# Kernel tuning notes

Measured on AMD Instinct MI355X. Metric: run time of the kernel, lower is better.

Reference implementation:

```python
import jax, jax.numpy as jnp
import numpy as np

B, T_IN, N, F_EMB = 64, 48, 64, 64
MAX_LEN = 64
H1 = 128   # rnn_1 hidden
H2 = 128   # rnn_2 hidden
HL = 128   # attribute_rnn (LSTM head) hidden
EMB = 32
VOCAB = 40
NC = 33    # len(unique_activities) + 1
IN_LSTM = H2 + EMB * 4  # rnn_2 + emb*(3 + attribute_number=1)


def setup_inputs():
    key = jax.random.key(0)
    ks = jax.random.split(key, 20)
    s = 0.05
    return {
        'concatenation': jax.random.normal(ks[0], (B, T_IN, N, F_EMB), jnp.float32),
        'A_in': jax.random.uniform(ks[1], (B, N, N), jnp.float32),
        'last_places_activated': jax.random.randint(ks[2], (B, 1), 0, N),
        'multiple_outputs': 0,
        'X_attributes': jax.random.randint(ks[3], (B, T_IN, 4), 0, 34),
        # GGRNN_1 (graph-gated GRU) params
        'W1': jax.random.normal(ks[4], (F_EMB, 3 * H1), jnp.float32) * s,
        'U1': jax.random.normal(ks[5], (H1, 3 * H1), jnp.float32) * s,
        'b1': jnp.zeros((3 * H1,), jnp.float32),
        # GGRNN_2 params
        'W2': jax.random.normal(ks[6], (H1, 3 * H2), jnp.float32) * s,
        'U2': jax.random.normal(ks[7], (H2, 3 * H2), jnp.float32) * s,
        'b2': jnp.zeros((3 * H2,), jnp.float32),
        # graph_embedder embedding tables
        'E_act': jax.random.normal(ks[8], (VOCAB, EMB), jnp.float32) * s,
        'E_t1': jax.random.normal(ks[9], (VOCAB, EMB), jnp.float32) * s,
        'E_t2': jax.random.normal(ks[10], (VOCAB, EMB), jnp.float32) * s,
        'E_attr': jax.random.normal(ks[11], (VOCAB, EMB), jnp.float32) * s,
        # LSTMHead params (1 layer LSTM + linear classifier)
        'Wx': jax.random.normal(ks[12], (IN_LSTM, 4 * HL), jnp.float32) * s,
        'Wh': jax.random.normal(ks[13], (HL, 4 * HL), jnp.float32) * s,
        'bl': jnp.zeros((4 * HL,), jnp.float32),
        'Wo': jax.random.normal(ks[14], (HL, NC), jnp.float32) * s,
        'bo': jnp.zeros((NC,), jnp.float32),
    }


def _ggrnn(x, A, W, U, b):
    # x: [B,T,N,F]; graph message passing (A @ x_t) feeding a per-node GRU over time
    H = U.shape[0]
    def step(h, x_t):              # h, x_t: [B,N,*]
        m = jnp.einsum('bij,bjf->bif', A, x_t)
        gx = m @ W + b             # [B,N,3H]
        gh = h @ U
        z = jax.nn.sigmoid(gx[..., :H] + gh[..., :H])
        r = jax.nn.sigmoid(gx[..., H:2 * H] + gh[..., H:2 * H])
        n = jnp.tanh(gx[..., 2 * H:] + r * gh[..., 2 * H:])
        h_new = (1.0 - z) * n + z * h
        return h_new, h_new
    h0 = jnp.zeros((x.shape[0], x.shape[2], H), x.dtype)
    _, hs = jax.lax.scan(step, h0, jnp.moveaxis(x, 1, 0))
    return jnp.moveaxis(hs, 0, 1)  # return_sequences -> [B,T,N,H]


def _lstm_head(x, Wx, Wh, b, Wo, bo):
    # x: [B,T,D] -> last hidden -> logits [B,NC]
    H = Wh.shape[0]
    def step(carry, x_t):
        h, c = carry
        g = x_t @ Wx + h @ Wh + b  # [B,4H]
        i = jax.nn.sigmoid(g[:, :H])
        f = jax.nn.sigmoid(g[:, H:2 * H])
        gg = jnp.tanh(g[:, 2 * H:3 * H])
        o = jax.nn.sigmoid(g[:, 3 * H:])
        c = f * c + i * gg
        h = o * jnp.tanh(c)
        return (h, c), None
    init = (jnp.zeros((x.shape[0], H), x.dtype), jnp.zeros((x.shape[0], H), x.dtype))
    (h, _), _ = jax.lax.scan(step, init, jnp.moveaxis(x, 1, 0))
    return h @ Wo + bo


def reference(concatenation, A_in, last_places_activated, multiple_outputs, X_attributes,
              W1, U1, b1, W2, U2, b2, E_act, E_t1, E_t2, E_attr, Wx, Wh, bl, Wo, bo):
    # zero-pad time dim at the FRONT to max_len (ZeroPad2d after permute)
    pad_t = MAX_LEN - concatenation.shape[1]
    x = jnp.pad(concatenation, ((0, 0), (pad_t, 0), (0, 0), (0, 0)))
    x = _ggrnn(x, A_in, W1, U1, b1)     # [B,T,N,H1]
    x = _ggrnn(x, A_in, W2, U2, b2)     # [B,T,N,H2]
    # the nested python loop reverses time, max-pools over nodes, and re-inserts at
    # the front, which exactly preserves time order -> plain segment max over N
    pooled = jnp.max(x, axis=2)         # [B,T,H2]
    # attribute embeddings (zero-index padding at the front of time)
    pad_a = MAX_LEN - X_attributes.shape[1]
    attrs = jnp.pad(X_attributes, ((0, 0), (pad_a, 0), (0, 0)))
    emb = jnp.concatenate([E_act[attrs[..., 0]], E_t1[attrs[..., 1]],
                           E_t2[attrs[..., 2]], E_attr[attrs[..., 3]]], axis=-1)
    seq = jnp.concatenate([pooled, emb], axis=-1)  # [B,T,H2+4*EMB]
    logits = _lstm_head(seq, Wx, Wh, bl, Wo, bo)   # [B,NC]
    return logits
```

## Files before the change

### kernel.cpp

```cpp
#include <hip/hip_runtime.h>
#include <hip/hip_bf16.h>
#include <cstdint>


#define BB 64
#define TIN 48
#define TPAD 16
#define G3 384
#define NC 33
#define HL4 512

using u16 = unsigned short;
using u32 = unsigned int;
using bf16x8 = __attribute__((ext_vector_type(8))) short;
using f32x4  = __attribute__((ext_vector_type(4))) float;

__device__ __forceinline__ float b2f(u16 u) {
    u32 x = ((u32)u) << 16; float f; __builtin_memcpy(&f, &x, 4); return f;
}
__device__ __forceinline__ u16 f2b(float f) {
    u32 x; __builtin_memcpy(&x, &f, 4);
    u32 r = (x + 0x7fffu + ((x >> 16) & 1u)) >> 16;
    return (u16)r;
}
__device__ __forceinline__ float sigm(float x) { return 1.f / (1.f + __expf(-x)); }
__device__ __forceinline__ float tanh_f(float x) {
    float e = __expf(2.f * x);
    return 1.f - 2.f / (e + 1.f);
}
__device__ __forceinline__ u32 encf(float f) {
    int i = __float_as_int(f);
    return (i < 0) ? ~(u32)i : ((u32)i | 0x80000000u);
}
__device__ __forceinline__ float decf(u32 u) {
    int i = (u & 0x80000000u) ? (int)(u & 0x7fffffffu) : ~(int)u;
    return __int_as_float(i);
}

__global__ __launch_bounds__(256) void prep_kernel(
        const float* __restrict__ A, const float* __restrict__ U1,
        const float* __restrict__ U2, const float* __restrict__ W1,
        const float* __restrict__ W2, const float* __restrict__ Wx,
        u16* __restrict__ ah, u16* __restrict__ al,
        u16* __restrict__ uth1, u16* __restrict__ uth2,
        u16* __restrict__ wth1, u16* __restrict__ wth2,
        u16* __restrict__ wxth, u16* __restrict__ wxtl) {
    int blk = blockIdx.x, tid = threadIdx.x;
    if (blk < 1024) {
        int idx = blk * 256 + tid;
        float f = A[idx];
        int bi = idx >> 6, j = idx & 63;
        int o = (bi << 6) + (j ^ ((bi & 7) << 3));
        u16 h = f2b(f); ah[o] = h; al[o] = f2b(f - b2f(h));
    } else if (blk < 1216) {
        int idx = (blk - 1024) * 256 + tid;
        int k = idx & 127, col = idx >> 7;
        uth1[col * 128 + k] = f2b(U1[(size_t)k * G3 + col]);
    } else if (blk < 1408) {
        int idx = (blk - 1216) * 256 + tid;
        int k = idx & 127, col = idx >> 7;
        uth2[col * 128 + k] = f2b(U2[(size_t)k * G3 + col]);
    } else if (blk < 1504) {
        int idx = (blk - 1408) * 256 + tid;
        int col = idx % 384, k = idx / 384;
        wth1[(size_t)col * 64 + k] = f2b(W1[(size_t)k * 384 + col]);
    } else if (blk < 1696) {
        int idx = (blk - 1504) * 256 + tid;
        int col = idx % 384, k = idx / 384;
        wth2[(size_t)col * 128 + k] = f2b(W2[(size_t)k * 384 + col]);
    } else {
        int idx = (blk - 1696) * 256 + tid;
        int col = idx & 511, k = idx >> 9;
        float f = Wx[(size_t)k * HL4 + col];
        u16 h = f2b(f);
        wxth[(size_t)col * 256 + k] = h;
        wxtl[(size_t)col * 256 + k] = f2b(f - b2f(h));
    }
}

template<int F>
__global__ __launch_bounds__(256, 4) void bmm_kernel(
        const u16* __restrict__ ah, const u16* __restrict__ al,
        const float* __restrict__ x1, const u16* __restrict__ h1,
        u16* __restrict__ mh, int T, int TPB) {
    __shared__ __align__(16) u16 Xs[F * 64];
    __shared__ float txf[(F == 64) ? 64 : 1][(F == 64) ? 65 : 1];
    __shared__ u16 txh[(F == 128) ? 64 : 1][(F == 128) ? 136 : 1];
    const int blk = blockIdx.x;
    const int b = blk & 63, tg0 = (blk >> 6) * TPB;
    const int tid = threadIdx.x;
    const int w = tid >> 6, l = tid & 63, lr = l & 15, lk = l >> 4;

    bf16x8 afh[2], afl[2];
    {
        int row = w * 16 + lr;
        #pragma unroll
        for (int ks = 0; ks < 2; ++ks) {
            int idx = (b << 12) + row * 64 + ((ks * 32 + lk * 8) ^ ((row & 7) << 3));
            afh[ks] = *(const bf16x8*)&ah[idx];
            afl[ks] = *(const bf16x8*)&al[idx];
        }
    }

    for (int it = 0; it < TPB; ++it) {
        const int tl = tg0 + it;
        __syncthreads();
        if constexpr (F == 64) {
            const float* in = x1 + (size_t)(b * TIN + tl) * 4096;
            for (int idx = tid; idx < 4096; idx += 256)
                txf[idx >> 6][idx & 63] = in[idx];
        } else {
            const uint4* in = (const uint4*)(h1 + (size_t)(b * TIN + tl) * 8192);
            for (int idx = tid; idx < 1024; idx += 256) {
                int j = idx >> 4, c8 = idx & 15;
                *(uint4*)&txh[j][c8 * 8] = in[idx];
            }
        }
        __syncthreads();
        if constexpr (F == 64) {
            #pragma unroll
            for (int it2 = 0; it2 < 2; ++it2) {
                int f = it2 * 32 + (tid >> 3), cc = tid & 7;
                int jb = (cc ^ (f & 7)) * 8;
                u16 tmp[8];
                #pragma unroll
                for (int jj = 0; jj < 8; ++jj) tmp[jj] = f2b(txf[jb + jj][f]);
                *(uint4*)&Xs[f * 64 + cc * 8] = *(uint4*)tmp;
            }
        } else {
            #pragma unroll
            for (int it2 = 0; it2 < 4; ++it2) {
                int d = it2 * 32 + (tid >> 3), cc = tid & 7;
                int jb = (cc ^ (d & 7)) * 8;
                u16 tmp[8];
                #pragma unroll
                for (int jj = 0; jj < 8; ++jj) tmp[jj] = txh[jb + jj][d];
                *(uint4*)&Xs[d * 64 + cc * 8] = *(uint4*)tmp;
            }
        }
        __syncthreads();

        constexpr int NCT = F / 16;
        f32x4 macc[NCT];
        #pragma unroll
        for (int ct = 0; ct < NCT; ++ct) macc[ct] = (f32x4){0.f, 0.f, 0.f, 0.f};
        #pragma unroll
        for (int ct = 0; ct < NCT; ++ct) {
            int f = ct * 16 + lr;
            #pragma unroll
            for (int ks = 0; ks < 2; ++ks) {
                bf16x8 xf = *(const bf16x8*)&Xs[f * 64 + ((ks * 32 + lk * 8) ^ ((f & 7) << 3))];
                macc[ct] = __builtin_amdgcn_mfma_f32_16x16x32_bf16(afh[ks], xf, macc[ct], 0, 0, 0);
                macc[ct] = __builtin_amdgcn_mfma_f32_16x16x32_bf16(afl[ks], xf, macc[ct], 0, 0, 0);
            }
        }
        u16* oh = mh + (size_t)(b * T + tl) * 64 * F;
        #pragma unroll
        for (int ct = 0; ct < NCT; ++ct)
            #pragma unroll
            for (int q = 0; q < 4; ++q) {
                int row = w * 16 + lk * 4 + q;
                int col = ct * 16 + lr;
                oh[row * F + col] = f2b(macc[ct][q]);
            }
    }
}

template<int F, bool POOL>
__global__ __launch_bounds__(512, 2) void scan_mfma_kernel(
        const u16* __restrict__ mh, const u16* __restrict__ uth,
        const u16* __restrict__ wth, const float* __restrict__ bias,
        u16* __restrict__ hout, u32* __restrict__ pooled, int S) {
    constexpr int KS = F / 32;
    constexpr int RQ = F / 8;
    __shared__ u16 hhi[2][16][136];
    __shared__ u16 msh[2][16][F + 8];
    const int tid = threadIdx.x;
    const int wave = tid >> 6, l = tid & 63;
    const int lr = l & 15, lk = l >> 4;
    const int blk = blockIdx.x;
    const int b = blk & 63;
    const int n0 = (blk >> 6) * 16;
    const int d = wave * 16 + lr;

    bf16x8 ub[3][4], wbh[3][KS];
    float bias3[3];
    #pragma unroll
    for (int g = 0; g < 3; ++g) {
        int col = g * 128 + d;
        #pragma unroll
        for (int ks = 0; ks < 4; ++ks)
            ub[g][ks] = *(const bf16x8*)&uth[col * 128 + ks * 32 + lk * 8];
        #pragma unroll
        for (int ks = 0; ks < KS; ++ks)
            wbh[g][ks] = *(const bf16x8*)&wth[(size_t)col * F + ks * 32 + lk * 8];
        bias3[g] = bias[col];
    }

    float hold[4] = {0.f, 0.f, 0.f, 0.f};
    #pragma unroll
    for (int q = 0; q < 4; ++q)
        hhi[0][lk * 4 + q][d] = 0;
    if (tid < 16 * RQ) {
        int row = tid / RQ, c8 = tid % RQ;
        uint4 v = *(const uint4*)&mh[((size_t)(b * S) * 64 + n0 + row) * F + c8 * 8];
        *(uint4*)&msh[0][row][c8 * 8] = v;
    }
    __syncthreads();

    for (int s = 0; s < S; ++s) {
        uint4 tv;
        const bool have = (s + 1 < S);
        if (have && tid < 16 * RQ) {
            int row = tid / RQ, c8 = tid % RQ;
            tv = *(const uint4*)&mh[((size_t)(b * S + s + 1) * 64 + n0 + row) * F + c8 * 8];
        }
        if (!POOL && s >= 1 && tid < 256) {
            int dr = tid >> 4, kb = tid & 15;
            uint4 v = *(const uint4*)&hhi[s & 1][dr][kb * 8];
            *(uint4*)(hout + ((size_t)(b * TIN + s - 1) * 64 + n0 + dr) * 128 + kb * 8) = v;
        }
        __builtin_amdgcn_s_setprio(1);
        f32x4 gxa[3];
        #pragma unroll
        for (int g = 0; g < 3; ++g)
            gxa[g] = (f32x4){bias3[g], bias3[g], bias3[g], bias3[g]};
        #pragma unroll
        for (int ks = 0; ks < KS; ++ks) {
            bf16x8 mhf = *(const bf16x8*)&msh[s & 1][lr][ks * 32 + lk * 8];
            #pragma unroll
            for (int g = 0; g < 3; ++g)
                gxa[g] = __builtin_amdgcn_mfma_f32_16x16x32_bf16(mhf, wbh[g][ks], gxa[g], 0, 0, 0);
        }
        f32x4 acc[3];
        acc[0] = acc[1] = acc[2] = (f32x4){0.f, 0.f, 0.f, 0.f};
        #pragma unroll
        for (int ks = 0; ks < 4; ++ks) {
            bf16x8 ahh = *(const bf16x8*)&hhi[s & 1][lr][ks * 32 + lk * 8];
            #pragma unroll
            for (int g = 0; g < 3; ++g)
                acc[g] = __builtin_amdgcn_mfma_f32_16x16x32_bf16(ahh, ub[g][ks], acc[g], 0, 0, 0);
        }
        __builtin_amdgcn_s_setprio(0);
        #pragma unroll
        for (int q = 0; q < 4; ++q) {
            float z  = sigm(gxa[0][q] + acc[0][q]);
            float r2 = sigm(gxa[1][q] + acc[1][q]);
            float nn = tanh_f(gxa[2][q] + r2 * acc[2][q]);
            float h = (1.f - z) * nn + z * hold[q];
            hold[q] = h;
            hhi[(s + 1) & 1][lk * 4 + q][d] = f2b(h);
        }
        if (POOL) {
            float mx = fmaxf(fmaxf(hold[0], hold[1]), fmaxf(hold[2], hold[3]));
            mx = fmaxf(mx, __shfl_xor(mx, 16, 64));
            mx = fmaxf(mx, __shfl_xor(mx, 32, 64));
            if (lk == 0)
                atomicMax(&pooled[((size_t)(b * 64 + TPAD + s)) * 128 + d], encf(mx));
        }
        if (have && tid < 16 * RQ) {
            int row = tid / RQ, c8 = tid % RQ;
            *(uint4*)&msh[(s + 1) & 1][row][c8 * 8] = tv;
        }
        __syncthreads();
    }

    if (!POOL && tid < 256) {
        int dr = tid >> 4, kb = tid & 15;
        uint4 v = *(const uint4*)&hhi[S & 1][dr][kb * 8];
        *(uint4*)(hout + ((size_t)(b * TIN + S - 1) * 64 + n0 + dr) * 128 + kb * 8) = v;
    }
}

__global__ __launch_bounds__(256, 2) void seqgemm_kernel(
        const u32* __restrict__ pooled, const int* __restrict__ xattr,
        const float* __restrict__ Ea, const float* __restrict__ E1,
        const float* __restrict__ E2, const float* __restrict__ E3,
        const u16* __restrict__ wxth, const u16* __restrict__ wxtl,
        const float* __restrict__ bl, float* __restrict__ gxl) {
    __shared__ __align__(16) u16 Ss[64 * 256];
    const int b = blockIdx.x;
    const int r0 = b * 64;
    const int c0 = blockIdx.y * 256;
    const int tid = threadIdx.x;
    const int w = tid >> 6, l = tid & 63, lr = l & 15, lk = l >> 4;
    const uint4* p4 = (const uint4*)pooled;
    for (int i = tid; i < 2048; i += 256) {
        int t = i >> 5, c4 = i & 31;
        uint4 e = p4[((size_t)(b * 64 + t)) * 32 + c4];
        u16 tmp[4];
        if (t < TPAD) { tmp[0] = tmp[1] = tmp[2] = tmp[3] = 0; }
        else {
            tmp[0] = f2b(decf(e.x)); tmp[1] = f2b(decf(e.y));
            tmp[2] = f2b(decf(e.z)); tmp[3] = f2b(decf(e.w));
        }
        *(uint2*)&Ss[t * 256 + ((c4 * 4) ^ ((t & 7) << 3))] = *(uint2*)tmp;
    }
    {
        int t = tid >> 2, tbl = tid & 3;
        int idx = (t >= TPAD) ? xattr[((size_t)(b * TIN + t - TPAD)) * 4 + tbl] : 0;
        const float* E = (tbl == 0) ? Ea : (tbl == 1) ? E1 : (tbl == 2) ? E2 : E3;
        const float4* E4 = (const float4*)(E + idx * 32);
        #pragma unroll
        for (int j = 0; j < 8; ++j) {
            float4 ev = E4[j];
            u16 tmp[4] = {f2b(ev.x), f2b(ev.y), f2b(ev.z), f2b(ev.w)};
            int col = 128 + tbl * 32 + j * 4;
            *(uint2*)&Ss[t * 256 + (col ^ ((t & 7) << 3))] = *(uint2*)tmp;
        }
    }
    __syncthreads();
    f32x4 acc[4][4];
    #pragma unroll
    for (int rt = 0; rt < 4; ++rt)
        #pragma unroll
        for (int ct = 0; ct < 4; ++ct) acc[rt][ct] = (f32x4){0.f, 0.f, 0.f, 0.f};
    const int cw = c0 + w * 64;
    #pragma unroll
    for (int ks = 0; ks < 8; ++ks) {
        bf16x8 af[4];
        #pragma unroll
        for (int rt = 0; rt < 4; ++rt) {
            int row = rt * 16 + lr;
            af[rt] = *(const bf16x8*)&Ss[row * 256 + ((ks * 32 + lk * 8) ^ ((row & 7) << 3))];
        }
        #pragma unroll
        for (int ct = 0; ct < 4; ++ct) {
            int col = cw + ct * 16 + lr;
            bf16x8 wfh = *(const bf16x8*)&wxth[(size_t)col * 256 + ks * 32 + lk * 8];
            bf16x8 wfl = *(const bf16x8*)&wxtl[(size_t)col * 256 + ks * 32 + lk * 8];
            #pragma unroll
            for (int rt = 0; rt < 4; ++rt) {
                acc[rt][ct] = __builtin_amdgcn_mfma_f32_16x16x32_bf16(af[rt], wfh, acc[rt][ct], 0, 0, 0);
                acc[rt][ct] = __builtin_amdgcn_mfma_f32_16x16x32_bf16(af[rt], wfl, acc[rt][ct], 0, 0, 0);
            }
        }
    }
    #pragma unroll
    for (int ct = 0; ct < 4; ++ct) {
        int col = cw + ct * 16 + lr;
        float bv = bl[col];
        #pragma unroll
        for (int rt = 0; rt < 4; ++rt)
            #pragma unroll
            for (int q = 0; q < 4; ++q) {
                int row = r0 + rt * 16 + lk * 4 + q;
                gxl[(size_t)row * HL4 + col] = acc[rt][ct][q] + bv;
            }
    }
}

__global__ __launch_bounds__(1024) void lstm_kernel(
        const float* __restrict__ gxl, const float* __restrict__ Wh,
        const float* __restrict__ Wo, const float* __restrict__ bo,
        float* __restrict__ out) {
    __shared__ float hsd[128];
    __shared__ __align__(16) float part[8][128][4];
    int b = blockIdx.x; int tid = threadIdx.x;
    int kq = tid >> 7, d = tid & 127;
    float w[4][16];
    #pragma unroll
    for (int g = 0; g < 4; ++g)
        #pragma unroll
        for (int kk = 0; kk < 16; ++kk)
            w[g][kk] = Wh[(size_t)(kq * 16 + kk) * HL4 + g * 128 + d];
    float c = 0.f;
    float gl[4];
    if (tid < 128) {
        hsd[tid] = 0.f;
        #pragma unroll
        for (int g = 0; g < 4; ++g)
            gl[g] = gxl[((size_t)(b * 64)) * HL4 + g * 128 + d];
    }
    __syncthreads();
    for (int t = 0; t < 64; ++t) {
        float a[4] = {0.f, 0.f, 0.f, 0.f};
        #pragma unroll
        for (int k4 = 0; k4 < 4; ++k4) {
            float4 hv = *(const float4*)&hsd[kq * 16 + k4 * 4];
            #pragma unroll
            for (int g = 0; g < 4; ++g) {
                a[g] += hv.x * w[g][k4 * 4 + 0] + hv.y * w[g][k4 * 4 + 1]
                      + hv.z * w[g][k4 * 4 + 2] + hv.w * w[g][k4 * 4 + 3];
            }
        }
        if (kq) {
            float4 pv = {a[0], a[1], a[2], a[3]};
            *(float4*)&part[kq][d][0] = pv;
        }
        __syncthreads();
        if (kq == 0) {
            float gsum[4] = {a[0], a[1], a[2], a[3]};
            #pragma unroll
            for (int q = 1; q < 8; ++q) {
                float4 v = *(const float4*)&part[q][d][0];
                gsum[0] += v.x; gsum[1] += v.y; gsum[2] += v.z; gsum[3] += v.w;
            }
            #pragma unroll
            for (int g = 0; g < 4; ++g) gsum[g] += gl[g];
            if (t + 1 < 64) {
                #pragma unroll
                for (int g = 0; g < 4; ++g)
                    gl[g] = gxl[((size_t)(b * 64 + t + 1)) * HL4 + g * 128 + d];
            }
            float ii = sigm(gsum[0]), ff = sigm(gsum[1]);
            float gg = tanh_f(gsum[2]), oo = sigm(gsum[3]);
            c = ff * c + ii * gg;
            hsd[d] = oo * tanh_f(c);
        }
        __syncthreads();
    }
    if (tid < NC) {
        float accv = bo[tid];
        for (int k = 0; k < 128; ++k) accv += hsd[k] * Wo[k * NC + tid];
        out[b * NC + tid] = accv;
    }
}

extern "C" void kernel_launch(void* const* d_in, const int* in_sizes, int n_in,
                              void* d_out, int out_size, void* d_ws, size_t ws_size,
                              hipStream_t stream) {
    const float* x  = (const float*)d_in[0];
    const float* A  = (const float*)d_in[1];
    const int* xattr = (const int*)d_in[4];
    const float* W1 = (const float*)d_in[5];
    const float* U1 = (const float*)d_in[6];
    const float* b1 = (const float*)d_in[7];
    const float* W2 = (const float*)d_in[8];
    const float* U2 = (const float*)d_in[9];
    const float* b2 = (const float*)d_in[10];
    const float* Ea = (const float*)d_in[11];
    const float* E1 = (const float*)d_in[12];
    const float* E2 = (const float*)d_in[13];
    const float* E3 = (const float*)d_in[14];
    const float* Wx = (const float*)d_in[15];
    const float* Wh = (const float*)d_in[16];
    const float* bl = (const float*)d_in[17];
    const float* Wo = (const float*)d_in[18];
    const float* bo = (const float*)d_in[19];
    float* out = (float*)d_out;
    char* ws = (char*)d_ws;
    u16* mh      = (u16*)(ws);
    u16* h1      = (u16*)(ws + 50331648);
    float* gxl   = (float*)(ws + 100663296);
    u16* a_hi    = (u16*)(ws + 109051904);
    u16* a_lo    = (u16*)(ws + 109576192);
    u16* wth1    = (u16*)(ws + 110100480);
    u16* wth2    = (u16*)(ws + 110149632);
    u16* uth1    = (u16*)(ws + 110247936);
    u16* uth2    = (u16*)(ws + 110346240);
    u16* wxth    = (u16*)(ws + 110444544);
    u16* wxtl    = (u16*)(ws + 110706688);
    u32* pooled  = (u32*)(ws + 110968832);

    prep_kernel<<<2208, 256, 0, stream>>>(A, U1, U2, W1, W2, Wx,
        a_hi, a_lo, uth1, uth2, wth1, wth2, wxth, wxtl);
    hipMemsetAsync(pooled, 0, 2097152, stream);

    bmm_kernel<64><<<BB * 12, 256, 0, stream>>>(a_hi, a_lo, x, nullptr, mh, 48, 4);
    scan_mfma_kernel<64, false><<<256, 512, 0, stream>>>(
        mh, uth1, wth1, b1, h1, nullptr, 48);
    bmm_kernel<128><<<BB * 16, 256, 0, stream>>>(a_hi, a_lo, nullptr, h1, mh, 48, 3);
    scan_mfma_kernel<128, true><<<256, 512, 0, stream>>>(
        mh, uth2, wth2, b2, nullptr, pooled, 48);
    seqgemm_kernel<<<dim3(64, 2), 256, 0, stream>>>(
        pooled, xattr, Ea, E1, E2, E3, wxth, wxtl, bl, gxl);
    lstm_kernel<<<64, 1024, 0, stream>>>(gxl, Wh, Wo, bo, out);
}
```

Measured before the change: 253.9 us.

## Fuse LSTM input projection into LSTM kernel and fold pooled memset into prep

Merges the sequence input-projection GEMM (pooled features plus embeddings times Wx) into the LSTM recurrence kernel, keeping the per-batch gate pre-activations in shared memory instead of writing and rereading a global buffer. The memset of the pooled buffer is replaced by extra blocks in the prep kernel. This removes two launches and a global round trip. In exchange, the GEMM now runs on only 64 blocks, each using about 130KB of shared memory, which limits how much of the GPU does that work.

```diff
diff --git a/kernel.cpp b/kernel.cpp
--- a/kernel.cpp
+++ b/kernel.cpp
@@ -44,7 +44,8 @@
         u16* __restrict__ ah, u16* __restrict__ al,
         u16* __restrict__ uth1, u16* __restrict__ uth2,
         u16* __restrict__ wth1, u16* __restrict__ wth2,
-        u16* __restrict__ wxth, u16* __restrict__ wxtl) {
+        u16* __restrict__ wxth, u16* __restrict__ wxtl,
+        u32* __restrict__ pooled) {
     int blk = blockIdx.x, tid = threadIdx.x;
     if (blk < 1024) {
         int idx = blk * 256 + tid;
@@ -68,13 +69,15 @@
         int idx = (blk - 1504) * 256 + tid;
         int col = idx % 384, k = idx / 384;
         wth2[(size_t)col * 128 + k] = f2b(W2[(size_t)k * 384 + col]);
-    } else {
+    } else if (blk < 2208) {
         int idx = (blk - 1696) * 256 + tid;
         int col = idx & 511, k = idx >> 9;
         float f = Wx[(size_t)k * HL4 + col];
         u16 h = f2b(f);
         wxth[(size_t)col * 256 + k] = h;
         wxtl[(size_t)col * 256 + k] = f2b(f - b2f(h));
+    } else {
+        pooled[(blk - 2208) * 256 + tid] = 0;
     }
 }
 
@@ -272,106 +275,85 @@
     }
 }
 
-__global__ __launch_bounds__(256, 2) void seqgemm_kernel(
+__global__ __launch_bounds__(1024, 1) void lstm_fused_kernel(
         const u32* __restrict__ pooled, const int* __restrict__ xattr,
         const float* __restrict__ Ea, const float* __restrict__ E1,
         const float* __restrict__ E2, const float* __restrict__ E3,
         const u16* __restrict__ wxth, const u16* __restrict__ wxtl,
-        const float* __restrict__ bl, float* __restrict__ gxl) {
-    __shared__ __align__(16) u16 Ss[64 * 256];
+        const float* __restrict__ bl, const float* __restrict__ Wh,
+        const float* __restrict__ Wo, const float* __restrict__ bo,
+        float* __restrict__ out) {
+    __shared__ float gxl[64][516];
+    __shared__ float hsd[128];
+    __shared__ __align__(16) float part[8][128][4];
     const int b = blockIdx.x;
-    const int r0 = b * 64;
-    const int c0 = blockIdx.y * 256;
     const int tid = threadIdx.x;
     const int w = tid >> 6, l = tid & 63, lr = l & 15, lk = l >> 4;
-    const uint4* p4 = (const uint4*)pooled;
-    for (int i = tid; i < 2048; i += 256) {
-        int t = i >> 5, c4 = i & 31;
-        uint4 e = p4[((size_t)(b * 64 + t)) * 32 + c4];
-        u16 tmp[4];
-        if (t < TPAD) { tmp[0] = tmp[1] = tmp[2] = tmp[3] = 0; }
-        else {
-            tmp[0] = f2b(decf(e.x)); tmp[1] = f2b(decf(e.y));
-            tmp[2] = f2b(decf(e.z)); tmp[3] = f2b(decf(e.w));
-        }
-        *(uint2*)&Ss[t * 256 + ((c4 * 4) ^ ((t & 7) << 3))] = *(uint2*)tmp;
-    }
+
     {
-        int t = tid >> 2, tbl = tid & 3;
-        int idx = (t >= TPAD) ? xattr[((size_t)(b * TIN + t - TPAD)) * 4 + tbl] : 0;
-        const float* E = (tbl == 0) ? Ea : (tbl == 1) ? E1 : (tbl == 2) ? E2 : E3;
-        const float4* E4 = (const float4*)(E + idx * 32);
-        #pragma unroll
-        for (int j = 0; j < 8; ++j) {
-            float4 ev = E4[j];
-            u16 tmp[4] = {f2b(ev.x), f2b(ev.y), f2b(ev.z), f2b(ev.w)};
-            int col = 128 + tbl * 32 + j * 4;
-            *(uint2*)&Ss[t * 256 + (col ^ ((t & 7) << 3))] = *(uint2*)tmp;
-        }
-    }
-    __syncthreads();
-    f32x4 acc[4][4];
-    #pragma unroll
-    for (int rt = 0; rt < 4; ++rt)
-        #pragma unroll
-        for (int ct = 0; ct < 4; ++ct) acc[rt][ct] = (f32x4){0.f, 0.f, 0.f, 0.f};
-    const int cw = c0 + w * 64;
-    #pragma unroll
-    for (int ks = 0; ks < 8; ++ks) {
-        bf16x8 af[4];
-        #pragma unroll
-        for (int rt = 0; rt < 4; ++rt) {
-            int row = rt * 16 + lr;
-            af[rt] = *(const bf16x8*)&Ss[row * 256 + ((ks * 32 + lk * 8) ^ ((row & 7) << 3))];
-        }
-        #pragma unroll
-        for (int ct = 0; ct < 4; ++ct) {
-            int col = cw + ct * 16 + lr;
-            bf16x8 wfh = *(const bf16x8*)&wxth[(size_t)col * 256 + ks * 32 + lk * 8];
-            bf16x8 wfl = *(const bf16x8*)&wxtl[(size_t)col * 256 + ks * 32 + lk * 8];
-            #pragma unroll
-            for (int rt = 0; rt < 4; ++rt) {
-                acc[rt][ct] = __builtin_amdgcn_mfma_f32_16x16x32_bf16(af[rt], wfh, acc[rt][ct], 0, 0, 0);
-                acc[rt][ct] = __builtin_amdgcn_mfma_f32_16x16x32_bf16(af[rt], wfl, acc[rt][ct], 0, 0, 0);
-            }
-        }
-    }
-    #pragma unroll
-    for (int ct = 0; ct < 4; ++ct) {
-        int col = cw + ct * 16 + lr;
-        float bv = bl[col];
-        #pragma unroll
-        for (int rt = 0; rt < 4; ++rt)
-            #pragma unroll
-            for (int q = 0; q < 4; ++q) {
-                int row = r0 + rt * 16 + lk * 4 + q;
-                gxl[(size_t)row * HL4 + col] = acc[rt][ct][q] + bv;
-            }
-    }
-}
-
-__global__ __launch_bounds__(1024) void lstm_kernel(
-        const float* __restrict__ gxl, const float* __restrict__ Wh,
-        const float* __restrict__ Wo, const float* __restrict__ bo,
-        float* __restrict__ out) {
-    __shared__ float hsd[128];
-    __shared__ __align__(16) float part[8][128][4];
-    int b = blockIdx.x; int tid = threadIdx.x;
+        const int t0 = (w & 3) * 16;
+        const int t = t0 + lr;
+        bf16x8 af[8];
+        #pragma unroll
+        for (int ks = 0; ks < 4; ++ks) {
+            int c0 = ks * 32 + lk * 8;
+            u16 tmp[8];
+            if (t < TPAD) {
+                #pragma unroll
+                for (int j = 0; j < 8; ++j) tmp[j] = 0;
+            } else {
+                const uint4* pp = (const uint4*)&pooled[((size_t)(b * 64 + t)) * 128 + c0];
+                uint4 e0 = pp[0], e1 = pp[1];
+                tmp[0] = f2b(decf(e0.x)); tmp[1] = f2b(decf(e0.y));
+                tmp[2] = f2b(decf(e0.z)); tmp[3] = f2b(decf(e0.w));
+                tmp[4] = f2b(decf(e1.x)); tmp[5] = f2b(decf(e1.y));
+                tmp[6] = f2b(decf(e1.z)); tmp[7] = f2b(decf(e1.w));
+            }
+            __builtin_memcpy(&af[ks], tmp, 16);
+        }
+        #pragma unroll
+        for (int ks = 4; ks < 8; ++ks) {
+            int c = ks * 32 + lk * 8 - 128;
+            int tbl = c >> 5, cc = c & 31;
+            int idx = (t >= TPAD) ? xattr[((size_t)(b * TIN + t - TPAD)) * 4 + tbl] : 0;
+            const float* E = (tbl == 0) ? Ea : (tbl == 1) ? E1 : (tbl == 2) ? E2 : E3;
+            float4 e0 = *(const float4*)&E[idx * 32 + cc];
+            float4 e1 = *(const float4*)&E[idx * 32 + cc + 4];
+            u16 tmp[8] = {f2b(e0.x), f2b(e0.y), f2b(e0.z), f2b(e0.w),
+                          f2b(e1.x), f2b(e1.y), f2b(e1.z), f2b(e1.w)};
+            __builtin_memcpy(&af[ks], tmp, 16);
+        }
+        const int ctbase = (w >> 2) * 8;
+        #pragma unroll
+        for (int ct = 0; ct < 8; ++ct) {
+            int col = (ctbase + ct) * 16 + lr;
+            f32x4 acc = (f32x4){0.f, 0.f, 0.f, 0.f};
+            #pragma unroll
+            for (int ks = 0; ks < 8; ++ks) {
+                bf16x8 wfh = *(const bf16x8*)&wxth[(size_t)col * 256 + ks * 32 + lk * 8];
+                acc = __builtin_amdgcn_mfma_f32_16x16x32_bf16(af[ks], wfh, acc, 0, 0, 0);
+            }
+            #pragma unroll
+            for (int ks = 0; ks < 8; ++ks) {
+                bf16x8 wfl = *(const bf16x8*)&wxtl[(size_t)col * 256 + ks * 32 + lk * 8];
+                acc = __builtin_amdgcn_mfma_f32_16x16x32_bf16(af[ks], wfl, acc, 0, 0, 0);
+            }
+            float bv = bl[col];
+            #pragma unroll
+            for (int q = 0; q < 4; ++q)
+                gxl[t0 + lk * 4 + q][col] = acc[q] + bv;
+        }
+    }
+
     int kq = tid >> 7, d = tid & 127;
-    float w[4][16];
+    float wreg[4][16];
     #pragma unroll
     for (int g = 0; g < 4; ++g)
         #pragma unroll
         for (int kk = 0; kk < 16; ++kk)
-            w[g][kk] = Wh[(size_t)(kq * 16 + kk) * HL4 + g * 128 + d];
+            wreg[g][kk] = Wh[(size_t)(kq * 16 + kk) * HL4 + g * 128 + d];
     float c = 0.f;
-    float gl[4];
-    if (tid < 128) {
-        hsd[tid] = 0.f;
-        #pragma unroll
-        for (int g = 0; g < 4; ++g)
-            gl[g] = gxl[((size_t)(b * 64)) * HL4 + g * 128 + d];
-    }
+    if (tid < 128) hsd[tid] = 0.f;
     __syncthreads();
     for (int t = 0; t < 64; ++t) {
         float a[4] = {0.f, 0.f, 0.f, 0.f};
@@ -380,8 +362,8 @@
             float4 hv = *(const float4*)&hsd[kq * 16 + k4 * 4];
             #pragma unroll
             for (int g = 0; g < 4; ++g) {
-                a[g] += hv.x * w[g][k4 * 4 + 0] + hv.y * w[g][k4 * 4 + 1]
-                      + hv.z * w[g][k4 * 4 + 2] + hv.w * w[g][k4 * 4 + 3];
+                a[g] += hv.x * wreg[g][k4 * 4 + 0] + hv.y * wreg[g][k4 * 4 + 1]
+                      + hv.z * wreg[g][k4 * 4 + 2] + hv.w * wreg[g][k4 * 4 + 3];
             }
         }
         if (kq) {
@@ -397,12 +379,7 @@
                 gsum[0] += v.x; gsum[1] += v.y; gsum[2] += v.z; gsum[3] += v.w;
             }
             #pragma unroll
-            for (int g = 0; g < 4; ++g) gsum[g] += gl[g];
-            if (t + 1 < 64) {
-                #pragma unroll
-                for (int g = 0; g < 4; ++g)
-                    gl[g] = gxl[((size_t)(b * 64 + t + 1)) * HL4 + g * 128 + d];
-            }
+            for (int g = 0; g < 4; ++g) gsum[g] += gxl[t][g * 128 + d];
             float ii = sigm(gsum[0]), ff = sigm(gsum[1]);
             float gg = tanh_f(gsum[2]), oo = sigm(gsum[3]);
             c = ff * c + ii * gg;
@@ -442,20 +419,18 @@
     char* ws = (char*)d_ws;
     u16* mh      = (u16*)(ws);
     u16* h1      = (u16*)(ws + 50331648);
-    float* gxl   = (float*)(ws + 100663296);
-    u16* a_hi    = (u16*)(ws + 109051904);
-    u16* a_lo    = (u16*)(ws + 109576192);
-    u16* wth1    = (u16*)(ws + 110100480);
-    u16* wth2    = (u16*)(ws + 110149632);
-    u16* uth1    = (u16*)(ws + 110247936);
-    u16* uth2    = (u16*)(ws + 110346240);
-    u16* wxth    = (u16*)(ws + 110444544);
-    u16* wxtl    = (u16*)(ws + 110706688);
-    u32* pooled  = (u32*)(ws + 110968832);
-
-    prep_kernel<<<2208, 256, 0, stream>>>(A, U1, U2, W1, W2, Wx,
-        a_hi, a_lo, uth1, uth2, wth1, wth2, wxth, wxtl);
-    hipMemsetAsync(pooled, 0, 2097152, stream);
+    u16* a_hi    = (u16*)(ws + 100663296);
+    u16* a_lo    = (u16*)(ws + 101187584);
+    u16* wth1    = (u16*)(ws + 101711872);
+    u16* wth2    = (u16*)(ws + 101761024);
+    u16* uth1    = (u16*)(ws + 101859328);
+    u16* uth2    = (u16*)(ws + 101957632);
+    u16* wxth    = (u16*)(ws + 102055936);
+    u16* wxtl    = (u16*)(ws + 102318080);
+    u32* pooled  = (u32*)(ws + 102580224);
+
+    prep_kernel<<<4256, 256, 0, stream>>>(A, U1, U2, W1, W2, Wx,
+        a_hi, a_lo, uth1, uth2, wth1, wth2, wxth, wxtl, pooled);
 
     bmm_kernel<64><<<BB * 12, 256, 0, stream>>>(a_hi, a_lo, x, nullptr, mh, 48, 4);
     scan_mfma_kernel<64, false><<<256, 512, 0, stream>>>(
@@ -463,7 +438,6 @@
     bmm_kernel<128><<<BB * 16, 256, 0, stream>>>(a_hi, a_lo, nullptr, h1, mh, 48, 3);
     scan_mfma_kernel<128, true><<<256, 512, 0, stream>>>(
         mh, uth2, wth2, b2, nullptr, pooled, 48);
-    seqgemm_kernel<<<dim3(64, 2), 256, 0, stream>>>(
-        pooled, xattr, Ea, E1, E2, E3, wxth, wxtl, bl, gxl);
-    lstm_kernel<<<64, 1024, 0, stream>>>(gxl, Wh, Wo, bo, out);
-}
+    lstm_fused_kernel<<<64, 1024, 0, stream>>>(
+        pooled, xattr, Ea, E1, E2, E3, wxth, wxtl, bl, Wh, Wo, bo, out);
+}
```

Result: slower. 301.4 us (+18.7%).
